# Kernel optimization log

Hardware: AMD Instinct MI355X
Metric: run time of the kernel (lower is better)

Reference implementation:

```python
import jax, jax.numpy as jnp
import numpy as np

B, H, W = 8, 640, 640
THRESH = 0.6       # self.threshold in Pnet_post
NMS_IOU = 0.3      # iou threshold passed in post_data_Pnet
MAX_DET = 128      # fixed detection budget (padded greedy NMS)


def _tffix(x):
    # tf fix(): floor toward zero
    return jnp.where(x >= 0, jnp.floor(x), jnp.ceil(x))


def _rec2square(rect):
    # rect: [N,5] (x1,y1,x2,y2,score) -> squared boxes
    x1, y1, x2, y2, s = rect[:, 0], rect[:, 1], rect[:, 2], rect[:, 3], rect[:, 4]
    w = x2 - x1
    h = y2 - y1
    l = jnp.maximum(w, h)
    nx1 = x1 + w * 0.5 - l * 0.5
    ny1 = y1 + h * 0.5 - l * 0.5
    return jnp.stack([nx1, ny1, nx1 + l, ny1 + l, s], axis=1)


def _greedy_nms(rect, valid):
    # rect: [N,5]; valid: [N] bool (score >= THRESH). Sequential greedy NMS
    # (highest score first, suppress iou > NMS_IOU), padded to MAX_DET rows.
    x1, y1, x2, y2 = rect[:, 0], rect[:, 1], rect[:, 2], rect[:, 3]
    area = (x2 - x1 + 1.0) * (y2 - y1 + 1.0)
    s0 = jnp.where(valid, rect[:, 4], -jnp.inf)

    def step(s, _):
        i = jnp.argmax(s)
        alive = jnp.isfinite(s[i])
        xx1 = jnp.maximum(x1[i], x1)
        yy1 = jnp.maximum(y1[i], y1)
        xx2 = jnp.minimum(x2[i], x2)
        yy2 = jnp.minimum(y2[i], y2)
        inter = jnp.maximum(0.0, xx2 - xx1 + 1.0) * jnp.maximum(0.0, yy2 - yy1 + 1.0)
        iou = inter / (area[i] + area - inter)
        s_next = jnp.where(iou > NMS_IOU, -jnp.inf, s).at[i].set(-jnp.inf)
        s_next = jnp.where(alive, s_next, s)
        return s_next, (i, alive)

    _, (picks, alive) = jax.lax.scan(step, s0, None, length=MAX_DET)
    out = rect[picks]                       # [MAX_DET,5]
    return jnp.where(alive[:, None], out, 0.0)


def _post_single(cls, roi, scale, h_raw, w_raw):
    # cls: [H,W,2], roi: [H,W,4], scale/h_raw/w_raw: scalars
    h, w = cls.shape[0], cls.shape[1]
    score = cls[:, :, 1].T                  # [W,H] == Cls_pro[...,0]
    offset = jnp.transpose(roi, (1, 0, 2))  # [W,H,4] == stacked dx1..dx4
    out_side = max(w, h)
    stride = 0.0 if out_side == 1 else (2.0 * out_side + 11.0 - 12.0) / (out_side - 1.0)
    sc = 1.0 / scale                        # scale arg of _cls_bb2rect is 1/scale
    ii = jnp.broadcast_to(jnp.arange(w, dtype=jnp.float32)[:, None], (w, h))
    jj = jnp.broadcast_to(jnp.arange(h, dtype=jnp.float32)[None, :], (w, h))
    idx = jnp.stack([ii, jj], axis=-1)      # [W,H,2] grid coords (thresh_index)
    bb1 = _tffix(stride * idx * sc)
    bb2 = _tffix((stride * idx + 11.0) * sc)
    box = jnp.concatenate([bb1, bb2], axis=-1) + offset * 12.0 * sc  # [W,H,4]
    rect = jnp.concatenate([box, score[..., None]], axis=-1).reshape(-1, 5)
    rect = _rec2square(rect)
    # pick_rect: clip to image, swap inverted corners
    x1 = jnp.maximum(0.0, rect[:, 0])
    y1 = jnp.maximum(0.0, rect[:, 1])
    x2 = jnp.minimum(w_raw, rect[:, 2])
    y2 = jnp.minimum(h_raw, rect[:, 3])
    inv = (x1 > x2) | (y1 > y2)
    fx1 = jnp.where(inv, jnp.minimum(x1, x2), x1)
    fy1 = jnp.where(inv, jnp.minimum(y1, y2), y1)
    fx2 = jnp.where(inv, jnp.maximum(x1, x2), x2)
    fy2 = jnp.where(inv, jnp.maximum(y1, y2), y2)
    pick = jnp.stack([fx1, fy1, fx2, fy2, rect[:, 4]], axis=1)
    valid = score.reshape(-1) >= THRESH     # dynamic threshold -> mask
    return _greedy_nms(pick, valid)


def setup_inputs() -> dict:
    key = jax.random.key(0)
    k1, k2, k3 = jax.random.split(key, 3)
    classifier = jax.random.uniform(k1, (B, H, W, 2), dtype=jnp.float32)
    bbox_regress = jax.random.normal(k2, (B, H, W, 4), dtype=jnp.float32) * 0.1
    scale = jax.random.uniform(k3, (B,), dtype=jnp.float32, minval=0.4, maxval=1.0)
    height_raw = jnp.full((B, 1), 1500.0, dtype=jnp.float32)
    width_raw = jnp.full((B, 1), 1500.0, dtype=jnp.float32)
    return {"classifier": classifier, "bbox_regress": bbox_regress,
            "scale": scale, "height_raw": height_raw, "width_raw": width_raw}


def reference(classifier, bbox_regress, scale, height_raw, width_raw):
    # -> [B, MAX_DET, 5]; rows beyond #detections are zero
    return jax.vmap(_post_single)(classifier, bbox_regress, scale,
                                  height_raw[:, 0], width_raw[:, 0])
```

## Files before the change

### kernel.cpp

```cpp
#include <hip/hip_runtime.h>

#define Bn 8
#define Hn 640
#define Wn 640
#define CELLS (Hn*Wn)
#define NBIN 1024
#define HB 16
#define CB 32
#define CAP 4096
#define KTGT 3584u
#define MAXD 128
#define STAGE 512

#define WS_PART_BYTE 64
#define WS_KEYS_BYTE (64 + Bn*HB*NBIN*2)

__global__ void k_hist(const float4* __restrict__ cls4, unsigned short* __restrict__ part) {
    __shared__ unsigned h[NBIN];
    int b = blockIdx.y, blk = blockIdx.x, tid = threadIdx.x;
    for (int p = tid; p < NBIN; p += 256) h[p] = 0u;
    __syncthreads();
    const float4* src = cls4 + ((size_t)b * CELLS + blk * (CELLS / HB)) / 2;
    for (int k = 0; k < (CELLS / HB / 2) / 256; ++k) {
        float4 v = src[k * 256 + tid];
        if (v.y >= 0.6f) {
            int bin = min((int)((v.y - 0.6f) * 2560.0f), NBIN - 1);
            atomicAdd(&h[bin], 1u);
        }
        if (v.w >= 0.6f) {
            int bin = min((int)((v.w - 0.6f) * 2560.0f), NBIN - 1);
            atomicAdd(&h[bin], 1u);
        }
    }
    __syncthreads();
    unsigned short* dst = part + (size_t)(b * HB + blk) * NBIN;
    for (int p = tid; p < NBIN; p += 256) dst[p] = (unsigned short)h[p];
}

__global__ void k_cut(const unsigned short* __restrict__ part, float* __restrict__ cut,
                      unsigned* __restrict__ cnt) {
    __shared__ unsigned h[NBIN];
    __shared__ int best;
    int b = blockIdx.x, tid = threadIdx.x;
    unsigned acc[NBIN / 256];
    for (int q = 0; q < NBIN / 256; ++q) acc[q] = 0u;
    for (int blk = 0; blk < HB; ++blk) {
        const unsigned short* src = part + (size_t)(b * HB + blk) * NBIN;
        for (int q = 0; q < NBIN / 256; ++q) acc[q] += src[q * 256 + tid];
    }
    for (int q = 0; q < NBIN / 256; ++q) h[q * 256 + tid] = acc[q];
    if (tid == 0) { best = 0; cnt[b] = 0u; }
    __syncthreads();
    for (int off = 1; off < NBIN; off <<= 1) {
        unsigned v[NBIN / 256];
        for (int q = 0; q < NBIN / 256; ++q) {
            int p = q * 256 + tid;
            v[q] = h[p] + ((p + off < NBIN) ? h[p + off] : 0u);
        }
        __syncthreads();
        for (int q = 0; q < NBIN / 256; ++q) h[q * 256 + tid] = v[q];
        __syncthreads();
    }
    for (int q = 0; q < NBIN / 256; ++q) {
        int p = q * 256 + tid;
        if (h[p] >= KTGT && (p == NBIN - 1 || h[p + 1] < KTGT)) best = p;
    }
    __syncthreads();
    if (tid == 0) cut[b] = 0.6f + (float)best * (0.4f / (float)NBIN);
}

__global__ void k_compact(const float4* __restrict__ cls4, const float* __restrict__ cut,
                          unsigned* __restrict__ cnt, unsigned long long* __restrict__ keys) {
    __shared__ unsigned long long buf[STAGE];
    __shared__ unsigned lcnt, gbase;
    int b = blockIdx.y, blk = blockIdx.x, tid = threadIdx.x;
    float c = cut[b];
    if (tid == 0) lcnt = 0u;
    __syncthreads();
    int cellbase = blk * (CELLS / CB);
    const float4* src = cls4 + ((size_t)b * CELLS + cellbase) / 2;
    for (int k = 0; k < (CELLS / CB / 2) / 256; ++k) {
        float4 v = src[k * 256 + tid];
        int mm = cellbase + (k * 256 + tid) * 2;
        #pragma unroll
        for (int c2 = 0; c2 < 2; ++c2) {
            float s = c2 ? v.w : v.y;
            if (s >= c) {
                unsigned idx = atomicAdd(&lcnt, 1u);
                if (idx < STAGE) {
                    int m2 = mm + c2;
                    int i = m2 % Wn, j = m2 / Wn;
                    unsigned n = (unsigned)(i * Hn + j);
                    buf[idx] = ((unsigned long long)__float_as_uint(s) << 32) |
                               (unsigned long long)(~n);
                }
            }
        }
    }
    __syncthreads();
    unsigned total = min(lcnt, (unsigned)STAGE);
    if (tid == 0) gbase = atomicAdd(&cnt[b], total);
    __syncthreads();
    unsigned gb = gbase;
    for (unsigned i = tid; i < total; i += 256) {
        unsigned slot = gb + i;
        if (slot < CAP) keys[(size_t)b * CAP + slot] = buf[i];
    }
}

__device__ __forceinline__ void make_box(int n, float sc, float WR, float HR,
                                         const float4* __restrict__ roi4b,
                                         float& fx1, float& fy1, float& fx2, float& fy2,
                                         float& area) {
    const float stride = (float)(1279.0 / 639.0);
    int i = n / Hn, j = n % Hn;
    float fi = (float)i, fj = (float)j;
    float b1x = truncf((stride * fi) * sc);
    float b1y = truncf((stride * fj) * sc);
    float b2x = truncf((stride * fi + 11.0f) * sc);
    float b2y = truncf((stride * fj + 11.0f) * sc);
    float4 off = roi4b[j * Wn + i];
    float x1 = b1x + (off.x * 12.0f) * sc;
    float y1 = b1y + (off.y * 12.0f) * sc;
    float x2 = b2x + (off.z * 12.0f) * sc;
    float y2 = b2y + (off.w * 12.0f) * sc;
    float w = x2 - x1, h = y2 - y1;
    float l = fmaxf(w, h);
    float nx1 = x1 + w * 0.5f - l * 0.5f;
    float ny1 = y1 + h * 0.5f - l * 0.5f;
    float nx2 = nx1 + l, ny2 = ny1 + l;
    float cx1 = fmaxf(0.0f, nx1), cy1 = fmaxf(0.0f, ny1);
    float cx2 = fminf(WR, nx2),   cy2 = fminf(HR, ny2);
    bool inv = (cx1 > cx2) || (cy1 > cy2);
    fx1 = inv ? fminf(cx1, cx2) : cx1;
    fy1 = inv ? fminf(cy1, cy2) : cy1;
    fx2 = inv ? fmaxf(cx1, cx2) : cx2;
    fy2 = inv ? fmaxf(cy1, cy2) : cy2;
    area = (fx2 - fx1 + 1.0f) * (fy2 - fy1 + 1.0f);
}

__device__ __forceinline__ void wave_phases(unsigned long long* ks, int chunkbase,
                                            int k, int jstart) {
    int lane = threadIdx.x & 63;
    for (int j = jstart; j > 0; j >>= 1) {
        #pragma unroll
        for (int e0 = 0; e0 < 256; e0 += 64) {
            int p = chunkbase + e0 + lane;
            int ixj = p ^ j;
            if (ixj > p) {
                unsigned long long a = ks[p], c = ks[ixj];
                bool descBlk = ((p & k) == 0);
                if (descBlk ? (a < c) : (a > c)) { ks[p] = c; ks[ixj] = a; }
            }
        }
        asm volatile("s_waitcnt lgkmcnt(0)" ::: "memory");
    }
}

__launch_bounds__(1024)
__global__ void k_nms(const float4* __restrict__ roi4, const float* __restrict__ scale,
                      const float* __restrict__ hraw, const float* __restrict__ wraw,
                      const unsigned* __restrict__ cnt,
                      const unsigned long long* __restrict__ keys_g,
                      float* __restrict__ out) {
    __shared__ unsigned long long ks[CAP];
    __shared__ float4 abox[MAXD];
    __shared__ float aarea[MAXD], ascore[MAXD];
    int b = blockIdx.x, tid = threadIdx.x;
    int mn = (int)min(cnt[b], (unsigned)CAP);
    for (int p = tid; p < CAP; p += 1024)
        ks[p] = (p < mn) ? keys_g[(size_t)b * CAP + p] : 0ULL;
    __syncthreads();

    int wave = tid >> 6;
    int chunkbase = wave * 256;

    for (int k = 2; k <= 256; k <<= 1)
        wave_phases(ks, chunkbase, k, k >> 1);
    __syncthreads();

    for (int k = 512; k <= CAP; k <<= 1) {
        for (int j = k >> 1; j >= 256; j >>= 1) {
            for (int p = tid; p < CAP; p += 1024) {
                int ixj = p ^ j;
                if (ixj > p) {
                    unsigned long long a = ks[p], c = ks[ixj];
                    bool descBlk = ((p & k) == 0);
                    if (descBlk ? (a < c) : (a > c)) { ks[p] = c; ks[ixj] = a; }
                }
            }
            __syncthreads();
        }
        wave_phases(ks, chunkbase, k, 128);
        __syncthreads();
    }

    if (tid < 64) {
        int lane = tid;
        float sc = 1.0f / scale[b];
        float WR = wraw[b], HR = hraw[b];
        const float4* roi4b = roi4 + (size_t)b * CELLS;
        int n_acc = 0, pos = 0;
        while (pos < mn && n_acc < MAXD) {
            int myp = pos + lane;
            bool has = myp < mn;
            unsigned long long key = has ? ks[myp] : 0ULL;
            float s = __uint_as_float((unsigned)(key >> 32));
            unsigned n = ~(unsigned)key;
            float fx1, fy1, fx2, fy2, area;
            make_box(has ? (int)n : 0, sc, WR, HR, roi4b, fx1, fy1, fx2, fy2, area);
            bool rejected = !has;
            for (int k2 = 0; k2 < n_acc; ++k2) {
                float4 bb = abox[k2];
                float va = aarea[k2];
                float iw = fminf(fx2, bb.z) - fmaxf(fx1, bb.x) + 1.0f;
                float ih = fminf(fy2, bb.w) - fmaxf(fy1, bb.y) + 1.0f;
                float inter = fmaxf(0.0f, iw) * fmaxf(0.0f, ih);
                float iou = inter / (area + va - inter);
                rejected |= (iou > 0.3f);
            }
            unsigned long long active = __ballot(!rejected);
            while (active && n_acc < MAXD) {
                int f = __ffsll(active) - 1;
                float bx1 = __shfl(fx1, f), by1 = __shfl(fy1, f);
                float bx2 = __shfl(fx2, f), by2 = __shfl(fy2, f);
                float bar = __shfl(area, f), bs = __shfl(s, f);
                if (lane == 0) {
                    abox[n_acc] = make_float4(bx1, by1, bx2, by2);
                    aarea[n_acc] = bar;
                    ascore[n_acc] = bs;
                }
                if (lane == f) rejected = true;
                if (!rejected) {
                    float iw = fminf(fx2, bx2) - fmaxf(fx1, bx1) + 1.0f;
                    float ih = fminf(fy2, by2) - fmaxf(fy1, by1) + 1.0f;
                    float inter = fmaxf(0.0f, iw) * fmaxf(0.0f, ih);
                    float iou = inter / (area + bar - inter);
                    rejected |= (iou > 0.3f);
                }
                n_acc++;
                active = __ballot(!rejected);
            }
            pos += 64;
        }
        for (int q = lane; q < MAXD * 5; q += 64) {
            int k2 = q / 5, c = q % 5;
            float v = 0.0f;
            if (k2 < n_acc) {
                float4 bb = abox[k2];
                v = (c == 0) ? bb.x : (c == 1) ? bb.y : (c == 2) ? bb.z
                    : (c == 3) ? bb.w : ascore[k2];
            }
            out[(b * MAXD + k2) * 5 + c] = v;
        }
    }
}

extern "C" void kernel_launch(void* const* d_in, const int* in_sizes, int n_in,
                              void* d_out, int out_size, void* d_ws, size_t ws_size,
                              hipStream_t stream) {
    const float4* cls4 = (const float4*)d_in[0];
    const float4* roi4 = (const float4*)d_in[1];
    const float* scale = (const float*)d_in[2];
    const float* hraw  = (const float*)d_in[3];
    const float* wraw  = (const float*)d_in[4];
    float* out = (float*)d_out;

    unsigned* cnt = (unsigned*)d_ws;
    float*    cut = (float*)((char*)d_ws + 32);
    unsigned short* part = (unsigned short*)((char*)d_ws + WS_PART_BYTE);
    unsigned long long* keys = (unsigned long long*)((char*)d_ws + WS_KEYS_BYTE);

    hipLaunchKernelGGL(k_hist, dim3(HB, Bn), dim3(256), 0, stream, cls4, part);
    hipLaunchKernelGGL(k_cut, dim3(Bn), dim3(256), 0, stream, part, cut, cnt);
    hipLaunchKernelGGL(k_compact, dim3(CB, Bn), dim3(256), 0, stream, cls4, cut, cnt, keys);
    hipLaunchKernelGGL(k_nms, dim3(Bn), dim3(1024), 0, stream,
                       roi4, scale, hraw, wraw, cnt, keys, out);
}
```

Measured before the change: 236.8 us.

## Split candidates into score tiers and sort/NMS tier by tier with early exit

```diff
diff --git a/kernel.cpp b/kernel.cpp
--- a/kernel.cpp
+++ b/kernel.cpp
@@ -4,16 +4,18 @@
 #define Hn 640
 #define Wn 640
 #define CELLS (Hn*Wn)
-#define NBIN 1024
+#define NBIN 2048
 #define HB 16
 #define CB 32
-#define CAP 4096
-#define KTGT 3584u
+#define NT 5
+#define TCAP 1024
+#define TSTEP 832u
 #define MAXD 128
-#define STAGE 512
-
-#define WS_PART_BYTE 64
-#define WS_KEYS_BYTE (64 + Bn*HB*NBIN*2)
+#define TSTAGE 192
+
+#define WS_CUT_BYTE 256
+#define WS_PART_BYTE 512
+#define WS_KEYS_BYTE (512 + Bn*HB*NBIN*2)
 
 __global__ void k_hist(const float4* __restrict__ cls4, unsigned short* __restrict__ part) {
     __shared__ unsigned h[NBIN];
@@ -24,11 +26,11 @@
     for (int k = 0; k < (CELLS / HB / 2) / 256; ++k) {
         float4 v = src[k * 256 + tid];
         if (v.y >= 0.6f) {
-            int bin = min((int)((v.y - 0.6f) * 2560.0f), NBIN - 1);
+            int bin = min((int)((v.y - 0.6f) * 5120.0f), NBIN - 1);
             atomicAdd(&h[bin], 1u);
         }
         if (v.w >= 0.6f) {
-            int bin = min((int)((v.w - 0.6f) * 2560.0f), NBIN - 1);
+            int bin = min((int)((v.w - 0.6f) * 5120.0f), NBIN - 1);
             atomicAdd(&h[bin], 1u);
         }
     }
@@ -37,45 +39,51 @@
     for (int p = tid; p < NBIN; p += 256) dst[p] = (unsigned short)h[p];
 }
 
-__global__ void k_cut(const unsigned short* __restrict__ part, float* __restrict__ cut,
+__global__ void k_cut(const unsigned short* __restrict__ part, float* __restrict__ cutv,
                       unsigned* __restrict__ cnt) {
     __shared__ unsigned h[NBIN];
-    __shared__ int best;
+    __shared__ int best[NT];
     int b = blockIdx.x, tid = threadIdx.x;
-    unsigned acc[NBIN / 256];
-    for (int q = 0; q < NBIN / 256; ++q) acc[q] = 0u;
+    const int Q = NBIN / 256;
+    unsigned acc[Q];
+    for (int q = 0; q < Q; ++q) acc[q] = 0u;
     for (int blk = 0; blk < HB; ++blk) {
         const unsigned short* src = part + (size_t)(b * HB + blk) * NBIN;
-        for (int q = 0; q < NBIN / 256; ++q) acc[q] += src[q * 256 + tid];
-    }
-    for (int q = 0; q < NBIN / 256; ++q) h[q * 256 + tid] = acc[q];
-    if (tid == 0) { best = 0; cnt[b] = 0u; }
+        for (int q = 0; q < Q; ++q) acc[q] += src[q * 256 + tid];
+    }
+    for (int q = 0; q < Q; ++q) h[q * 256 + tid] = acc[q];
+    if (tid < NT) best[tid] = 0;
+    if (tid < 8) cnt[b * 8 + tid] = 0u;
     __syncthreads();
     for (int off = 1; off < NBIN; off <<= 1) {
-        unsigned v[NBIN / 256];
-        for (int q = 0; q < NBIN / 256; ++q) {
+        unsigned v[Q];
+        for (int q = 0; q < Q; ++q) {
             int p = q * 256 + tid;
             v[q] = h[p] + ((p + off < NBIN) ? h[p + off] : 0u);
         }
         __syncthreads();
-        for (int q = 0; q < NBIN / 256; ++q) h[q * 256 + tid] = v[q];
+        for (int q = 0; q < Q; ++q) h[q * 256 + tid] = v[q];
         __syncthreads();
     }
-    for (int q = 0; q < NBIN / 256; ++q) {
-        int p = q * 256 + tid;
-        if (h[p] >= KTGT && (p == NBIN - 1 || h[p + 1] < KTGT)) best = p;
-    }
-    __syncthreads();
-    if (tid == 0) cut[b] = 0.6f + (float)best * (0.4f / (float)NBIN);
-}
-
-__global__ void k_compact(const float4* __restrict__ cls4, const float* __restrict__ cut,
+    for (int t = 0; t < NT; ++t) {
+        unsigned tgt = TSTEP * (unsigned)(t + 1);
+        for (int q = 0; q < Q; ++q) {
+            int p = q * 256 + tid;
+            if (h[p] >= tgt && (p == NBIN - 1 || h[p + 1] < tgt)) best[t] = p;
+        }
+    }
+    __syncthreads();
+    if (tid < NT) cutv[b * 8 + tid] = 0.6f + (float)best[tid] * (0.4f / (float)NBIN);
+}
+
+__global__ void k_compact(const float4* __restrict__ cls4, const float* __restrict__ cutv_g,
                           unsigned* __restrict__ cnt, unsigned long long* __restrict__ keys) {
-    __shared__ unsigned long long buf[STAGE];
-    __shared__ unsigned lcnt, gbase;
+    __shared__ unsigned long long buf[NT][TSTAGE];
+    __shared__ unsigned lcnt[NT], gbase[NT];
     int b = blockIdx.y, blk = blockIdx.x, tid = threadIdx.x;
-    float c = cut[b];
-    if (tid == 0) lcnt = 0u;
+    float c0 = cutv_g[b * 8 + 0], c1 = cutv_g[b * 8 + 1], cmid = cutv_g[b * 8 + 2],
+          c3 = cutv_g[b * 8 + 3], c4 = cutv_g[b * 8 + 4];
+    if (tid < NT) lcnt[tid] = 0u;
     __syncthreads();
     int cellbase = blk * (CELLS / CB);
     const float4* src = cls4 + ((size_t)b * CELLS + cellbase) / 2;
@@ -83,28 +91,31 @@
         float4 v = src[k * 256 + tid];
         int mm = cellbase + (k * 256 + tid) * 2;
         #pragma unroll
-        for (int c2 = 0; c2 < 2; ++c2) {
-            float s = c2 ? v.w : v.y;
-            if (s >= c) {
-                unsigned idx = atomicAdd(&lcnt, 1u);
-                if (idx < STAGE) {
-                    int m2 = mm + c2;
+        for (int half = 0; half < 2; ++half) {
+            float s = half ? v.w : v.y;
+            if (s >= c4) {
+                int t = (s < c0) + (s < c1) + (s < cmid) + (s < c3);
+                unsigned idx = atomicAdd(&lcnt[t], 1u);
+                if (idx < TSTAGE) {
+                    int m2 = mm + half;
                     int i = m2 % Wn, j = m2 / Wn;
                     unsigned n = (unsigned)(i * Hn + j);
-                    buf[idx] = ((unsigned long long)__float_as_uint(s) << 32) |
-                               (unsigned long long)(~n);
+                    buf[t][idx] = ((unsigned long long)__float_as_uint(s) << 32) |
+                                  (unsigned long long)(~n);
                 }
             }
         }
     }
     __syncthreads();
-    unsigned total = min(lcnt, (unsigned)STAGE);
-    if (tid == 0) gbase = atomicAdd(&cnt[b], total);
-    __syncthreads();
-    unsigned gb = gbase;
-    for (unsigned i = tid; i < total; i += 256) {
-        unsigned slot = gb + i;
-        if (slot < CAP) keys[(size_t)b * CAP + slot] = buf[i];
+    if (tid < NT) gbase[tid] = atomicAdd(&cnt[b * 8 + tid], min(lcnt[tid], (unsigned)TSTAGE));
+    __syncthreads();
+    for (int t = 0; t < NT; ++t) {
+        unsigned tot = min(lcnt[t], (unsigned)TSTAGE);
+        for (unsigned i = tid; i < tot; i += 256) {
+            unsigned slot = gbase[t] + i;
+            if (slot < TCAP)
+                keys[((size_t)b * NT + t) * TCAP + slot] = buf[t][i];
+        }
     }
 }
 
@@ -139,19 +150,16 @@
     area = (fx2 - fx1 + 1.0f) * (fy2 - fy1 + 1.0f);
 }
 
-__device__ __forceinline__ void wave_phases(unsigned long long* ks, int chunkbase,
-                                            int k, int jstart) {
+__device__ __forceinline__ void wave_phases64(unsigned long long* ks, int chunkbase,
+                                              int k, int jstart) {
     int lane = threadIdx.x & 63;
     for (int j = jstart; j > 0; j >>= 1) {
-        #pragma unroll
-        for (int e0 = 0; e0 < 256; e0 += 64) {
-            int p = chunkbase + e0 + lane;
-            int ixj = p ^ j;
-            if (ixj > p) {
-                unsigned long long a = ks[p], c = ks[ixj];
-                bool descBlk = ((p & k) == 0);
-                if (descBlk ? (a < c) : (a > c)) { ks[p] = c; ks[ixj] = a; }
-            }
+        int p = chunkbase + lane;
+        int ixj = p ^ j;
+        if (ixj > p) {
+            unsigned long long a = ks[p], c = ks[ixj];
+            bool descBlk = ((p & k) == 0);
+            if (descBlk ? (a < c) : (a > c)) { ks[p] = c; ks[ixj] = a; }
         }
         asm volatile("s_waitcnt lgkmcnt(0)" ::: "memory");
     }
@@ -163,86 +171,101 @@
                       const unsigned* __restrict__ cnt,
                       const unsigned long long* __restrict__ keys_g,
                       float* __restrict__ out) {
-    __shared__ unsigned long long ks[CAP];
+    __shared__ unsigned long long ks[TCAP];
     __shared__ float4 abox[MAXD];
     __shared__ float aarea[MAXD], ascore[MAXD];
+    __shared__ int sn_acc;
     int b = blockIdx.x, tid = threadIdx.x;
-    int mn = (int)min(cnt[b], (unsigned)CAP);
-    for (int p = tid; p < CAP; p += 1024)
-        ks[p] = (p < mn) ? keys_g[(size_t)b * CAP + p] : 0ULL;
-    __syncthreads();
-
-    int wave = tid >> 6;
-    int chunkbase = wave * 256;
-
-    for (int k = 2; k <= 256; k <<= 1)
-        wave_phases(ks, chunkbase, k, k >> 1);
-    __syncthreads();
-
-    for (int k = 512; k <= CAP; k <<= 1) {
-        for (int j = k >> 1; j >= 256; j >>= 1) {
-            for (int p = tid; p < CAP; p += 1024) {
-                int ixj = p ^ j;
-                if (ixj > p) {
-                    unsigned long long a = ks[p], c = ks[ixj];
-                    bool descBlk = ((p & k) == 0);
-                    if (descBlk ? (a < c) : (a > c)) { ks[p] = c; ks[ixj] = a; }
+    int wave = tid >> 6, lane = tid & 63;
+    int chunkbase = wave * 64;
+
+    if (tid == 0) sn_acc = 0;
+
+    int n_acc = 0;
+    float sc = 0.f, WR = 0.f, HR = 0.f;
+    const float4* roi4b = roi4;
+    if (tid < 64) {
+        sc = 1.0f / scale[b];
+        WR = wraw[b]; HR = hraw[b];
+        roi4b = roi4 + (size_t)b * CELLS;
+    }
+
+    for (int t = 0; t < NT; ++t) {
+        __syncthreads();
+        if (sn_acc >= MAXD) break;
+        int mt = (int)min(cnt[b * 8 + t], (unsigned)TCAP);
+        ks[tid] = (tid < mt) ? keys_g[((size_t)b * NT + t) * TCAP + tid] : 0ULL;
+        __syncthreads();
+
+        if (mt > 1) {
+            for (int k = 2; k <= 64; k <<= 1)
+                wave_phases64(ks, chunkbase, k, k >> 1);
+            __syncthreads();
+            for (int k = 128; k <= TCAP; k <<= 1) {
+                for (int j = k >> 1; j >= 64; j >>= 1) {
+                    int p = tid, ixj = p ^ j;
+                    if (ixj > p) {
+                        unsigned long long a = ks[p], c = ks[ixj];
+                        bool descBlk = ((p & k) == 0);
+                        if (descBlk ? (a < c) : (a > c)) { ks[p] = c; ks[ixj] = a; }
+                    }
+                    __syncthreads();
                 }
+                wave_phases64(ks, chunkbase, k, 32);
+                __syncthreads();
             }
-            __syncthreads();
-        }
-        wave_phases(ks, chunkbase, k, 128);
-        __syncthreads();
-    }
-
-    if (tid < 64) {
-        int lane = tid;
-        float sc = 1.0f / scale[b];
-        float WR = wraw[b], HR = hraw[b];
-        const float4* roi4b = roi4 + (size_t)b * CELLS;
-        int n_acc = 0, pos = 0;
-        while (pos < mn && n_acc < MAXD) {
-            int myp = pos + lane;
-            bool has = myp < mn;
-            unsigned long long key = has ? ks[myp] : 0ULL;
-            float s = __uint_as_float((unsigned)(key >> 32));
-            unsigned n = ~(unsigned)key;
-            float fx1, fy1, fx2, fy2, area;
-            make_box(has ? (int)n : 0, sc, WR, HR, roi4b, fx1, fy1, fx2, fy2, area);
-            bool rejected = !has;
-            for (int k2 = 0; k2 < n_acc; ++k2) {
-                float4 bb = abox[k2];
-                float va = aarea[k2];
-                float iw = fminf(fx2, bb.z) - fmaxf(fx1, bb.x) + 1.0f;
-                float ih = fminf(fy2, bb.w) - fmaxf(fy1, bb.y) + 1.0f;
-                float inter = fmaxf(0.0f, iw) * fmaxf(0.0f, ih);
-                float iou = inter / (area + va - inter);
-                rejected |= (iou > 0.3f);
-            }
-            unsigned long long active = __ballot(!rejected);
-            while (active && n_acc < MAXD) {
-                int f = __ffsll(active) - 1;
-                float bx1 = __shfl(fx1, f), by1 = __shfl(fy1, f);
-                float bx2 = __shfl(fx2, f), by2 = __shfl(fy2, f);
-                float bar = __shfl(area, f), bs = __shfl(s, f);
-                if (lane == 0) {
-                    abox[n_acc] = make_float4(bx1, by1, bx2, by2);
-                    aarea[n_acc] = bar;
-                    ascore[n_acc] = bs;
-                }
-                if (lane == f) rejected = true;
-                if (!rejected) {
-                    float iw = fminf(fx2, bx2) - fmaxf(fx1, bx1) + 1.0f;
-                    float ih = fminf(fy2, by2) - fmaxf(fy1, by1) + 1.0f;
+        }
+
+        if (tid < 64 && mt > 0) {
+            int pos = 0;
+            while (pos < mt && n_acc < MAXD) {
+                int myp = pos + lane;
+                bool has = myp < mt;
+                unsigned long long key = has ? ks[myp] : 0ULL;
+                float s = __uint_as_float((unsigned)(key >> 32));
+                unsigned n = ~(unsigned)key;
+                float fx1, fy1, fx2, fy2, area;
+                make_box(has ? (int)n : 0, sc, WR, HR, roi4b, fx1, fy1, fx2, fy2, area);
+                bool rejected = !has;
+                for (int k2 = 0; k2 < n_acc; ++k2) {
+                    float4 bb = abox[k2];
+                    float va = aarea[k2];
+                    float iw = fminf(fx2, bb.z) - fmaxf(fx1, bb.x) + 1.0f;
+                    float ih = fminf(fy2, bb.w) - fmaxf(fy1, bb.y) + 1.0f;
                     float inter = fmaxf(0.0f, iw) * fmaxf(0.0f, ih);
-                    float iou = inter / (area + bar - inter);
+                    float iou = inter / (area + va - inter);
                     rejected |= (iou > 0.3f);
                 }
-                n_acc++;
-                active = __ballot(!rejected);
+                unsigned long long active = __ballot(!rejected);
+                while (active && n_acc < MAXD) {
+                    int f = __ffsll(active) - 1;
+                    float bx1 = __shfl(fx1, f), by1 = __shfl(fy1, f);
+                    float bx2 = __shfl(fx2, f), by2 = __shfl(fy2, f);
+                    float bar = __shfl(area, f), bs = __shfl(s, f);
+                    if (lane == 0) {
+                        abox[n_acc] = make_float4(bx1, by1, bx2, by2);
+                        aarea[n_acc] = bar;
+                        ascore[n_acc] = bs;
+                    }
+                    if (lane == f) rejected = true;
+                    if (!rejected) {
+                        float iw = fminf(fx2, bx2) - fmaxf(fx1, bx1) + 1.0f;
+                        float ih = fminf(fy2, by2) - fmaxf(fy1, by1) + 1.0f;
+                        float inter = fmaxf(0.0f, iw) * fmaxf(0.0f, ih);
+                        float iou = inter / (area + bar - inter);
+                        rejected |= (iou > 0.3f);
+                    }
+                    n_acc++;
+                    active = __ballot(!rejected);
+                }
+                pos += 64;
             }
-            pos += 64;
-        }
+            if (tid == 0) sn_acc = n_acc;
+        }
+    }
+    __syncthreads();
+
+    if (tid < 64) {
         for (int q = lane; q < MAXD * 5; q += 64) {
             int k2 = q / 5, c = q % 5;
             float v = 0.0f;
@@ -267,13 +290,13 @@
     float* out = (float*)d_out;
 
     unsigned* cnt = (unsigned*)d_ws;
-    float*    cut = (float*)((char*)d_ws + 32);
+    float*    cutv = (float*)((char*)d_ws + WS_CUT_BYTE);
     unsigned short* part = (unsigned short*)((char*)d_ws + WS_PART_BYTE);
     unsigned long long* keys = (unsigned long long*)((char*)d_ws + WS_KEYS_BYTE);
 
     hipLaunchKernelGGL(k_hist, dim3(HB, Bn), dim3(256), 0, stream, cls4, part);
-    hipLaunchKernelGGL(k_cut, dim3(Bn), dim3(256), 0, stream, part, cut, cnt);
-    hipLaunchKernelGGL(k_compact, dim3(CB, Bn), dim3(256), 0, stream, cls4, cut, cnt, keys);
+    hipLaunchKernelGGL(k_cut, dim3(Bn), dim3(256), 0, stream, part, cutv, cnt);
+    hipLaunchKernelGGL(k_compact, dim3(CB, Bn), dim3(256), 0, stream, cls4, cutv, cnt, keys);
     hipLaunchKernelGGL(k_nms, dim3(Bn), dim3(1024), 0, stream,
                        roi4, scale, hraw, wraw, cnt, keys, out);
 }
```

Measured after the change: 205.8 us. -13.1%, faster.
